# Kernel tuning notes

Hardware: AMD Instinct MI355X
Metric: run time of the kernel (lower is better)

The kernel has to match this reference:

```python
import jax, jax.numpy as jnp
import numpy as np

B, L, D = 8, 2048, 256
D_MODEL = 1024
NUM_SIGNALS = 16
MAX_POSITIONS = 4096
ROLE_OUTPUT = 2  # role id used for the CLS token


def setup_inputs() -> dict:
    key = jax.random.key(0)
    ks = jax.random.split(key, 12)
    emb = jax.random.normal(ks[0], (B, L, D), dtype=jnp.float32)
    pos = jax.random.randint(ks[1], (B, L), 1, MAX_POSITIONS + 1)          # pos >= 1 for real tokens
    sid = jax.random.randint(ks[2], (B, L), 0, NUM_SIGNALS)
    role = jax.random.randint(ks[3], (B, L), 0, 3)
    padding_mask = jax.random.uniform(ks[4], (B, L)) < 0.75                # True = real token
    # learned parameters
    proj_W = jax.random.normal(ks[5], (NUM_SIGNALS, D_MODEL, D), dtype=jnp.float32) * (1.0 / np.sqrt(D))
    proj_b = jax.random.normal(ks[6], (NUM_SIGNALS, D_MODEL), dtype=jnp.float32) * 0.01
    cls_content = jax.random.normal(ks[7], (D_MODEL,), dtype=jnp.float32)
    pos_embed = jax.random.normal(ks[8], (MAX_POSITIONS + 1, D_MODEL), dtype=jnp.float32)
    id_embed = jax.random.normal(ks[9], (NUM_SIGNALS + 1, D_MODEL), dtype=jnp.float32)
    role_embed = jax.random.normal(ks[10], (3, D_MODEL), dtype=jnp.float32)
    return dict(emb=emb, pos=pos, sid=sid, role=role, padding_mask=padding_mask,
                proj_W=proj_W, proj_b=proj_b, cls_content=cls_content,
                pos_embed=pos_embed, id_embed=id_embed, role_embed=role_embed)


def reference(emb, pos, sid, role, padding_mask,
              proj_W, proj_b, cls_content, pos_embed, id_embed, role_embed):
    Bv, Lv, _ = emb.shape
    S, d_model, _ = proj_W.shape
    cls_id = S

    # Grouped per-signal projection: one GEMM per signal id, select per token.
    tokens = jnp.zeros((Bv, Lv, d_model), dtype=emb.dtype)
    for s in range(S):
        proj_s = jnp.einsum('bld,ed->ble', emb, proj_W[s]) + proj_b[s]   # (B, L, d_model)
        keep = ((sid == s) & padding_mask)[..., None]
        tokens = jnp.where(keep, proj_s, tokens)

    # Prepend CLS
    cls = jnp.broadcast_to(cls_content[None, None, :], (Bv, 1, d_model))
    tokens = jnp.concatenate([cls, tokens], axis=1)                       # (B, L+1, d_model)

    pos_full = jnp.concatenate([jnp.zeros((Bv, 1), dtype=pos.dtype), pos], axis=1)
    sid_full = jnp.concatenate([jnp.full((Bv, 1), cls_id, dtype=sid.dtype), sid], axis=1)
    role_full = jnp.concatenate([jnp.full((Bv, 1), ROLE_OUTPUT, dtype=role.dtype), role], axis=1)

    tokens = tokens + pos_embed[pos_full] + id_embed[sid_full] + role_embed[role_full]

    attn_keep = jnp.concatenate([jnp.ones((Bv, 1), dtype=bool), padding_mask], axis=1)
    return tokens, attn_keep
```

## Files before the change

### kernel.cpp

```cpp
#include <hip/hip_runtime.h>
#include <hip/hip_bf16.h>
#include <stdint.h>

#define B_ 8
#define L_ 2048
#define NTOK 16384
#define DK 256
#define DM 1024
#define NS 16
#define LOUT 2049
#define TOK_OUT (B_*LOUT*DM)
#define ATTN_OUT (B_*LOUT)
#define PCAP 2048

typedef unsigned short u16;
typedef unsigned int u32;
typedef __bf16 bf16x8 __attribute__((ext_vector_type(8)));
typedef float f32x4 __attribute__((ext_vector_type(4)));

__device__ inline float bf2f(u16 u) {
    u32 x = ((u32)u) << 16;
    float f;
    __builtin_memcpy(&f, &x, 4);
    return f;
}

__device__ inline u32 packbf2(float lo, float hi) {
    u32 a, b;
    __builtin_memcpy(&a, &lo, 4);
    __builtin_memcpy(&b, &hi, 4);
    a = (a + 0x8000u) >> 16;
    b = (b + 0x8000u) & 0xFFFF0000u;
    return a | b;
}

__device__ inline void gll16(const void* g, void* l) {
    __builtin_amdgcn_global_load_lds(
        (const __attribute__((address_space(1))) unsigned int*)g,
        (__attribute__((address_space(3))) unsigned int*)l, 16, 0, 0);
}

#define WS_CUR 0
#define WS_PERM 64
#define WS_MASK (64 + NS * PCAP)
#define EMB_OFF 262144ULL
#define W_OFF (EMB_OFF + 16384ULL * 512ULL)
#define WS_NEED (W_OFF + 16384ULL * 512ULL)

__global__ __launch_bounds__(256) void prep_all(
    const unsigned char* __restrict__ mb, const int* __restrict__ sid,
    const float* __restrict__ emb, const float* __restrict__ W,
    int* __restrict__ wsi, unsigned char* __restrict__ wsb) {
    __shared__ int f_c1ge2, f_ge2, f_odd;
    __shared__ int lcnt[NS], gbase[NS];
    int bid = blockIdx.x;
    int tid = threadIdx.x;

    if (bid < 64) {
        if (tid == 0) { f_c1ge2 = 0; f_ge2 = 0; f_odd = 0; }
        if (tid < NS) lcnt[tid] = 0;
        __syncthreads();

        int c1ge2 = 0, ge2 = 0, oddnz = 0;
        const u32* mw = (const u32*)mb;
        #pragma unroll
        for (int i = 0; i < 16; i++) {
            u32 x = mw[tid * 16 + i];
            u32 b0 = x & 0xFF, b1 = (x >> 8) & 0xFF, b2 = (x >> 16) & 0xFF, b3 = x >> 24;
            if (b1 >= 2) c1ge2 = 1;
            if (b0 >= 2 || b1 >= 2 || b2 >= 2 || b3 >= 2) ge2 = 1;
            if ((b1 | b3) != 0) oddnz = 1;
        }
        if (c1ge2) atomicOr(&f_c1ge2, 1);
        if (ge2) atomicOr(&f_ge2, 1);
        if (oddnz) atomicOr(&f_odd, 1);
        __syncthreads();

        int width;
        if (f_c1ge2) width = 2;
        else if (f_ge2) width = 4;
        else if (f_odd) width = 1;
        else width = 4;

        int t = bid * 256 + tid;
        int m;
        if (width == 1) m = (mb[t] != 0);
        else if (width == 2) m = (((const u16*)mb)[t] != 0);
        else m = (((const u32*)mb)[t] != 0);

        wsi[WS_MASK + t] = m;
        int s = sid[t];
        int lr = 0;
        if (m) lr = atomicAdd(&lcnt[s], 1);
        __syncthreads();
        if (tid < NS) gbase[tid] = atomicAdd(&wsi[WS_CUR + tid], lcnt[tid]);
        __syncthreads();
        if (m) {
            int r = gbase[s] + lr;
            if (r < PCAP) wsi[WS_PERM + s * PCAP + r] = t;
        }
        return;
    }

    int cb = bid - 64;
    int lane = tid & 63;
    int wv = tid >> 6;
    const float* src;
    u16* dst;
    if (cb < 4096) {
        src = emb;
        dst = (u16*)(wsb + EMB_OFF);
    } else {
        cb -= 4096;
        src = W;
        dst = (u16*)(wsb + W_OFF);
    }
    int r = cb * 4 + wv;
    float4 a = *(const float4*)(src + (size_t)r * DK + lane * 4);
    uint2 o;
    o.x = packbf2(a.x, a.y);
    o.y = packbf2(a.z, a.w);
    *(uint2*)(dst + (size_t)r * DK + lane * 4) = o;
}

__global__ __launch_bounds__(512, 4) void fused_main(
    const int* __restrict__ pos, const int* __restrict__ sid,
    const int* __restrict__ role,
    const float* __restrict__ bias, const float* __restrict__ cls,
    const float* __restrict__ pos_emb, const float* __restrict__ id_emb,
    const float* __restrict__ role_emb,
    const int* __restrict__ wsi, const unsigned char* __restrict__ wsb,
    float* __restrict__ out) {
    __shared__ u16 As[2][128 * 32];
    __shared__ u16 Bs[2][256 * 32];
    __shared__ int toks[128];
    int bi = (int)blockIdx.x;
    int tid = threadIdx.x;
    int lane = tid & 63;
    int wv = tid >> 6;

    if (bi >= 576) {
        int eb = bi - 576;
        if (eb < NTOK / 8) {
            int t = eb * 8 + wv;
            if (wsi[WS_MASK + t]) return;
            int p = pos[t], sd = sid[t], ro = role[t];
            int b = t >> 11, l = t & 2047;
            size_t orow = (size_t)(b * LOUT + l + 1) * DM;
            #pragma unroll
            for (int it = 0; it < 4; it++) {
                int c = it * 256 + lane * 4;
                f32x4 a = *(const f32x4*)(pos_emb + (size_t)p * DM + c);
                f32x4 d = *(const f32x4*)(id_emb + (size_t)sd * DM + c);
                f32x4 e = *(const f32x4*)(role_emb + (size_t)ro * DM + c);
                f32x4 o = a + d + e;
                __builtin_nontemporal_store(o, (f32x4*)(out + orow + c));
            }
        } else if (eb == NTOK / 8) {
            int b = wv;
            size_t orow = (size_t)(b * LOUT) * DM;
            #pragma unroll
            for (int it = 0; it < 4; it++) {
                int c = it * 256 + lane * 4;
                f32x4 cc = *(const f32x4*)(cls + c);
                f32x4 a = *(const f32x4*)(pos_emb + c);
                f32x4 d = *(const f32x4*)(id_emb + NS * DM + c);
                f32x4 e = *(const f32x4*)(role_emb + 2 * DM + c);
                f32x4 o = cc + a + d + e;
                *(f32x4*)(out + orow + c) = o;
            }
        } else {
            int i = (eb - NTOK / 8 - 1) * 512 + tid;
            if (i < ATTN_OUT) {
                int b = i / LOUT;
                int j = i - b * LOUT;
                float val = (j == 0) ? 1.0f : (float)wsi[WS_MASK + b * L_ + j - 1];
                out[TOK_OUT + i] = val;
            }
        }
        return;
    }

    int cnts[NS];
    int mtot = 0;
    #pragma unroll
    for (int i = 0; i < NS; i++) {
        int c = wsi[WS_CUR + i];
        cnts[i] = c > PCAP ? PCAP : c;
        mtot += (cnts[i] + 127) >> 7;
    }
    int xcd = bi & 7;
    int j = bi >> 3;
    int m_lo = (xcd * mtot) >> 3;
    int m_hi = ((xcd + 1) * mtot) >> 3;
    int cm = m_hi - m_lo;
    if (cm <= 0 || j >= cm * 4) return;
    int nt = j / cm;
    int m = m_lo + (j - nt * cm);
    int n0 = nt << 8;

    int s = -1, lrt = 0;
    #pragma unroll
    for (int i = 0; i < NS; i++) {
        int rt = (cnts[i] + 127) >> 7;
        if (s < 0) {
            if (m < rt) { s = i; lrt = m; }
            else m -= rt;
        }
    }
    if (s < 0) return;
    int rowsValid = cnts[s] - lrt * 128;
    if (rowsValid > 128) rowsValid = 128;

    if (tid < 128) {
        int base = WS_PERM + s * PCAP + lrt * 128;
        toks[tid] = wsi[base + ((tid < rowsValid) ? tid : 0)];
    }
    __syncthreads();

    const u16* Eb = (const u16*)(wsb + EMB_OFF);
    const u16* Bb = (const u16*)(wsb + W_OFF) + (size_t)(s * DM + n0) * DK;

    int srow = lane >> 2;
    int slseg = lane & 3;
    int arow = wv * 16 + srow;
    int ags = (slseg - (arow >> 1)) & 3;
    int brow1 = 128 + arow;
    int bgs1 = (slseg - (brow1 >> 1)) & 3;
    const u16* Asrc = Eb + (size_t)toks[arow] * DK;

    f32x4 acc[4][4];
    #pragma unroll
    for (int im = 0; im < 4; im++)
        #pragma unroll
        for (int jn = 0; jn < 4; jn++) acc[im][jn] = (f32x4){0.f, 0.f, 0.f, 0.f};

    int wm = wv & 1, wn = wv >> 1;
    int mcol = lane & 15;
    int quad = lane >> 4;

#define STAGE(kc, bf)                                                          \
    {                                                                          \
        gll16(Asrc + (kc) * 32 + ags * 8, &As[bf][wv * 16 * 32]);              \
        gll16(Bb + (size_t)arow * DK + (kc) * 32 + ags * 8,                    \
              &Bs[bf][wv * 16 * 32]);                                          \
        gll16(Bb + (size_t)brow1 * DK + (kc) * 32 + bgs1 * 8,                  \
              &Bs[bf][(128 + wv * 16) * 32]);                                  \
    }

    STAGE(0, 0)
    #pragma unroll
    for (int kc = 0; kc < 8; ++kc) {
        __syncthreads();
        if (kc < 7) STAGE(kc + 1, (kc + 1) & 1)
        int bf = kc & 1;
        bf16x8 af[4], bfr[4];
        #pragma unroll
        for (int im = 0; im < 4; im++) {
            int row = wm * 64 + im * 16 + mcol;
            int sg = (quad + (row >> 1)) & 3;
            af[im] = *(const bf16x8*)(&As[bf][row * 32 + sg * 8]);
        }
        #pragma unroll
        for (int jn = 0; jn < 4; jn++) {
            int row = wn * 64 + jn * 16 + mcol;
            int sg = (quad + (row >> 1)) & 3;
            bfr[jn] = *(const bf16x8*)(&Bs[bf][row * 32 + sg * 8]);
        }
        #pragma unroll
        for (int im = 0; im < 4; im++)
            #pragma unroll
            for (int jn = 0; jn < 4; jn++)
                acc[im][jn] = __builtin_amdgcn_mfma_f32_16x16x32_bf16(
                    af[im], bfr[jn], acc[im][jn], 0, 0, 0);
    }

    float bc[4];
    #pragma unroll
    for (int jn = 0; jn < 4; jn++) {
        int col = n0 + wn * 64 + jn * 16 + mcol;
        bc[jn] = bias[s * DM + col] + id_emb[s * DM + col];
    }
    #pragma unroll
    for (int im = 0; im < 4; im++) {
        #pragma unroll
        for (int r = 0; r < 4; r++) {
            int rowT = wm * 64 + im * 16 + quad * 4 + r;
            if (rowT >= rowsValid) continue;
            int t = toks[rowT];
            int p = pos[t];
            int ro = role[t];
            int b = t >> 11, l = t & 2047;
            size_t orow = (size_t)(b * LOUT + l + 1) * DM;
            const float* prow = pos_emb + (size_t)p * DM;
            #pragma unroll
            for (int jn = 0; jn < 4; jn++) {
                int col = n0 + wn * 64 + jn * 16 + mcol;
                float val = acc[im][jn][r] + bc[jn]
                    + prow[col]
                    + role_emb[ro * DM + col];
                __builtin_nontemporal_store(val, &out[orow + col]);
            }
        }
    }
#undef STAGE
}

extern "C" void kernel_launch(void* const* d_in, const int* in_sizes, int n_in,
                              void* d_out, int out_size, void* d_ws, size_t ws_size,
                              hipStream_t stream) {
    const float* emb = (const float*)d_in[0];
    const int* pos = (const int*)d_in[1];
    const int* sid = (const int*)d_in[2];
    const int* role = (const int*)d_in[3];
    const unsigned char* mask = (const unsigned char*)d_in[4];
    const float* W = (const float*)d_in[5];
    const float* bias = (const float*)d_in[6];
    const float* cls = (const float*)d_in[7];
    const float* pos_emb = (const float*)d_in[8];
    const float* id_emb = (const float*)d_in[9];
    const float* role_emb = (const float*)d_in[10];
    float* out = (float*)d_out;
    int* wsi = (int*)d_ws;
    unsigned char* wsb = (unsigned char*)d_ws;

    (void)hipMemsetAsync(wsi, 0, 64 * sizeof(int), stream);
    hipLaunchKernelGGL(prep_all, dim3(64 + 8192), dim3(256), 0, stream,
                       mask, sid, emb, W, wsi, wsb);
    hipLaunchKernelGGL(fused_main, dim3(576 + 2048 + 1 + 33), dim3(512), 0, stream,
                       pos, sid, role, bias, cls, pos_emb, id_emb, role_emb,
                       wsi, wsb, out);
}
```

Before: 154.1 us.

## Move masked-token, CLS and attention-mask writes into prep kernel

The elementwise output work (padded-token embedding sums, CLS rows, attention-keep mask) moves out of the GEMM kernel and into the prep kernel. Each of those blocks re-sniffs the mask width on its own, so the workspace mask array is no longer needed. The bf16 conversion blocks now handle four rows per wave instead of one, which cuts the conversion grid from 8192 to 2048 blocks. The aim is to overlap the bandwidth-bound writes with the conversion and leave the second kernel purely GEMM, at the cost of every elementwise block re-reading 16KB of mask.

```diff
diff --git a/kernel.cpp b/kernel.cpp
--- a/kernel.cpp
+++ b/kernel.cpp
@@ -18,13 +18,6 @@
 typedef __bf16 bf16x8 __attribute__((ext_vector_type(8)));
 typedef float f32x4 __attribute__((ext_vector_type(4)));
 
-__device__ inline float bf2f(u16 u) {
-    u32 x = ((u32)u) << 16;
-    float f;
-    __builtin_memcpy(&f, &x, 4);
-    return f;
-}
-
 __device__ inline u32 packbf2(float lo, float hi) {
     u32 a, b;
     __builtin_memcpy(&a, &lo, 4);
@@ -42,53 +35,67 @@
 
 #define WS_CUR 0
 #define WS_PERM 64
-#define WS_MASK (64 + NS * PCAP)
 #define EMB_OFF 262144ULL
 #define W_OFF (EMB_OFF + 16384ULL * 512ULL)
 #define WS_NEED (W_OFF + 16384ULL * 512ULL)
 
+__device__ inline int sniff_width(const unsigned char* mb, int tid, int* sh) {
+    if (tid == 0) { sh[0] = 0; sh[1] = 0; sh[2] = 0; }
+    __syncthreads();
+    int c1ge2 = 0, ge2 = 0, oddnz = 0;
+    const u32* mw = (const u32*)mb;
+    #pragma unroll
+    for (int i = 0; i < 16; i++) {
+        u32 x = mw[tid * 16 + i];
+        u32 b0 = x & 0xFF, b1 = (x >> 8) & 0xFF, b2 = (x >> 16) & 0xFF, b3 = x >> 24;
+        if (b1 >= 2) c1ge2 = 1;
+        if (b0 >= 2 || b1 >= 2 || b2 >= 2 || b3 >= 2) ge2 = 1;
+        if ((b1 | b3) != 0) oddnz = 1;
+    }
+    if (c1ge2) atomicOr(&sh[0], 1);
+    if (ge2) atomicOr(&sh[1], 1);
+    if (oddnz) atomicOr(&sh[2], 1);
+    __syncthreads();
+    if (sh[0]) return 2;
+    if (sh[1]) return 4;
+    if (sh[2]) return 1;
+    return 4;
+}
+
+__device__ inline int decode_mask(const unsigned char* mb, int t, int width) {
+    if (width == 1) return mb[t] != 0;
+    if (width == 2) return ((const u16*)mb)[t] != 0;
+    return ((const u32*)mb)[t] != 0;
+}
+
+#define SORT_B 64
+#define CONV_B 2048
+#define EW_B 4096
+#define EW0 (SORT_B + CONV_B)
+#define CLS0 (EW0 + EW_B)
+#define ATTN0 (CLS0 + 2)
+#define PREP_GRID (ATTN0 + 65)
+
 __global__ __launch_bounds__(256) void prep_all(
     const unsigned char* __restrict__ mb, const int* __restrict__ sid,
+    const int* __restrict__ pos, const int* __restrict__ role,
     const float* __restrict__ emb, const float* __restrict__ W,
-    int* __restrict__ wsi, unsigned char* __restrict__ wsb) {
-    __shared__ int f_c1ge2, f_ge2, f_odd;
+    const float* __restrict__ cls, const float* __restrict__ pos_emb,
+    const float* __restrict__ id_emb, const float* __restrict__ role_emb,
+    int* __restrict__ wsi, unsigned char* __restrict__ wsb,
+    float* __restrict__ out) {
+    __shared__ int sh[3];
     __shared__ int lcnt[NS], gbase[NS];
     int bid = blockIdx.x;
     int tid = threadIdx.x;
-
-    if (bid < 64) {
-        if (tid == 0) { f_c1ge2 = 0; f_ge2 = 0; f_odd = 0; }
+    int lane = tid & 63;
+    int wv = tid >> 6;
+
+    if (bid < SORT_B) {
         if (tid < NS) lcnt[tid] = 0;
-        __syncthreads();
-
-        int c1ge2 = 0, ge2 = 0, oddnz = 0;
-        const u32* mw = (const u32*)mb;
-        #pragma unroll
-        for (int i = 0; i < 16; i++) {
-            u32 x = mw[tid * 16 + i];
-            u32 b0 = x & 0xFF, b1 = (x >> 8) & 0xFF, b2 = (x >> 16) & 0xFF, b3 = x >> 24;
-            if (b1 >= 2) c1ge2 = 1;
-            if (b0 >= 2 || b1 >= 2 || b2 >= 2 || b3 >= 2) ge2 = 1;
-            if ((b1 | b3) != 0) oddnz = 1;
-        }
-        if (c1ge2) atomicOr(&f_c1ge2, 1);
-        if (ge2) atomicOr(&f_ge2, 1);
-        if (oddnz) atomicOr(&f_odd, 1);
-        __syncthreads();
-
-        int width;
-        if (f_c1ge2) width = 2;
-        else if (f_ge2) width = 4;
-        else if (f_odd) width = 1;
-        else width = 4;
-
+        int width = sniff_width(mb, tid, sh);
         int t = bid * 256 + tid;
-        int m;
-        if (width == 1) m = (mb[t] != 0);
-        else if (width == 2) m = (((const u16*)mb)[t] != 0);
-        else m = (((const u32*)mb)[t] != 0);
-
-        wsi[WS_MASK + t] = m;
+        int m = decode_mask(mb, t, width);
         int s = sid[t];
         int lr = 0;
         if (m) lr = atomicAdd(&lcnt[s], 1);
@@ -102,31 +109,85 @@
         return;
     }
 
-    int cb = bid - 64;
-    int lane = tid & 63;
-    int wv = tid >> 6;
-    const float* src;
-    u16* dst;
-    if (cb < 4096) {
-        src = emb;
-        dst = (u16*)(wsb + EMB_OFF);
-    } else {
-        cb -= 4096;
-        src = W;
-        dst = (u16*)(wsb + W_OFF);
-    }
-    int r = cb * 4 + wv;
-    float4 a = *(const float4*)(src + (size_t)r * DK + lane * 4);
-    uint2 o;
-    o.x = packbf2(a.x, a.y);
-    o.y = packbf2(a.z, a.w);
-    *(uint2*)(dst + (size_t)r * DK + lane * 4) = o;
-}
-
-__global__ __launch_bounds__(512, 4) void fused_main(
-    const int* __restrict__ pos, const int* __restrict__ sid,
-    const int* __restrict__ role,
-    const float* __restrict__ bias, const float* __restrict__ cls,
+    if (bid < EW0) {
+        int cb = bid - SORT_B;
+        const float* src;
+        u16* dst;
+        if (cb < 1024) {
+            src = emb;
+            dst = (u16*)(wsb + EMB_OFF);
+        } else {
+            cb -= 1024;
+            src = W;
+            dst = (u16*)(wsb + W_OFF);
+        }
+        int r0 = cb * 16 + wv * 4;
+        #pragma unroll
+        for (int i = 0; i < 4; i++) {
+            int r = r0 + i;
+            float4 a = *(const float4*)(src + (size_t)r * DK + lane * 4);
+            uint2 o;
+            o.x = packbf2(a.x, a.y);
+            o.y = packbf2(a.z, a.w);
+            *(uint2*)(dst + (size_t)r * DK + lane * 4) = o;
+        }
+        return;
+    }
+
+    if (bid < CLS0) {
+        int width = sniff_width(mb, tid, sh);
+        int t = (bid - EW0) * 4 + wv;
+        if (decode_mask(mb, t, width)) return;
+        int p = pos[t], sd = sid[t], ro = role[t];
+        int b = t >> 11, l = t & 2047;
+        size_t orow = (size_t)(b * LOUT + l + 1) * DM;
+        const float* pr = pos_emb + (size_t)p * DM;
+        const float* ir = id_emb + (size_t)sd * DM;
+        const float* rr = role_emb + (size_t)ro * DM;
+        #pragma unroll
+        for (int it = 0; it < 4; it++) {
+            int c = it * 256 + lane * 4;
+            f32x4 a = *(const f32x4*)(pr + c);
+            f32x4 d = *(const f32x4*)(ir + c);
+            f32x4 e = *(const f32x4*)(rr + c);
+            f32x4 o = a + d + e;
+            __builtin_nontemporal_store(o, (f32x4*)(out + orow + c));
+        }
+        return;
+    }
+
+    if (bid < ATTN0) {
+        int b = (bid - CLS0) * 4 + wv;
+        size_t orow = (size_t)(b * LOUT) * DM;
+        #pragma unroll
+        for (int it = 0; it < 4; it++) {
+            int c = it * 256 + lane * 4;
+            f32x4 cc = *(const f32x4*)(cls + c);
+            f32x4 a = *(const f32x4*)(pos_emb + c);
+            f32x4 d = *(const f32x4*)(id_emb + NS * DM + c);
+            f32x4 e = *(const f32x4*)(role_emb + 2 * DM + c);
+            f32x4 o = cc + a + d + e;
+            *(f32x4*)(out + orow + c) = o;
+        }
+        return;
+    }
+
+    {
+        int width = sniff_width(mb, tid, sh);
+        int i = (bid - ATTN0) * 256 + tid;
+        if (i < ATTN_OUT) {
+            int b = i / LOUT;
+            int j = i - b * LOUT;
+            float val = (j == 0) ? 1.0f
+                                 : (float)decode_mask(mb, b * L_ + j - 1, width);
+            out[TOK_OUT + i] = val;
+        }
+    }
+}
+
+__global__ __launch_bounds__(512, 4) void gemm_big(
+    const int* __restrict__ pos, const int* __restrict__ role,
+    const float* __restrict__ bias,
     const float* __restrict__ pos_emb, const float* __restrict__ id_emb,
     const float* __restrict__ role_emb,
     const int* __restrict__ wsi, const unsigned char* __restrict__ wsb,
@@ -138,48 +199,6 @@
     int tid = threadIdx.x;
     int lane = tid & 63;
     int wv = tid >> 6;
-
-    if (bi >= 576) {
-        int eb = bi - 576;
-        if (eb < NTOK / 8) {
-            int t = eb * 8 + wv;
-            if (wsi[WS_MASK + t]) return;
-            int p = pos[t], sd = sid[t], ro = role[t];
-            int b = t >> 11, l = t & 2047;
-            size_t orow = (size_t)(b * LOUT + l + 1) * DM;
-            #pragma unroll
-            for (int it = 0; it < 4; it++) {
-                int c = it * 256 + lane * 4;
-                f32x4 a = *(const f32x4*)(pos_emb + (size_t)p * DM + c);
-                f32x4 d = *(const f32x4*)(id_emb + (size_t)sd * DM + c);
-                f32x4 e = *(const f32x4*)(role_emb + (size_t)ro * DM + c);
-                f32x4 o = a + d + e;
-                __builtin_nontemporal_store(o, (f32x4*)(out + orow + c));
-            }
-        } else if (eb == NTOK / 8) {
-            int b = wv;
-            size_t orow = (size_t)(b * LOUT) * DM;
-            #pragma unroll
-            for (int it = 0; it < 4; it++) {
-                int c = it * 256 + lane * 4;
-                f32x4 cc = *(const f32x4*)(cls + c);
-                f32x4 a = *(const f32x4*)(pos_emb + c);
-                f32x4 d = *(const f32x4*)(id_emb + NS * DM + c);
-                f32x4 e = *(const f32x4*)(role_emb + 2 * DM + c);
-                f32x4 o = cc + a + d + e;
-                *(f32x4*)(out + orow + c) = o;
-            }
-        } else {
-            int i = (eb - NTOK / 8 - 1) * 512 + tid;
-            if (i < ATTN_OUT) {
-                int b = i / LOUT;
-                int j = i - b * LOUT;
-                float val = (j == 0) ? 1.0f : (float)wsi[WS_MASK + b * L_ + j - 1];
-                out[TOK_OUT + i] = val;
-            }
-        }
-        return;
-    }
 
     int cnts[NS];
     int mtot = 0;
@@ -325,9 +344,10 @@
     unsigned char* wsb = (unsigned char*)d_ws;
 
     (void)hipMemsetAsync(wsi, 0, 64 * sizeof(int), stream);
-    hipLaunchKernelGGL(prep_all, dim3(64 + 8192), dim3(256), 0, stream,
-                       mask, sid, emb, W, wsi, wsb);
-    hipLaunchKernelGGL(fused_main, dim3(576 + 2048 + 1 + 33), dim3(512), 0, stream,
-                       pos, sid, role, bias, cls, pos_emb, id_emb, role_emb,
+    hipLaunchKernelGGL(prep_all, dim3(PREP_GRID), dim3(256), 0, stream,
+                       mask, sid, pos, role, emb, W, cls, pos_emb, id_emb,
+                       role_emb, wsi, wsb, out);
+    hipLaunchKernelGGL(gemm_big, dim3(576), dim3(512), 0, stream,
+                       pos, role, bias, pos_emb, id_emb, role_emb,
                        wsi, wsb, out);
 }
```

After: 156.6 us. About the same (+1.6%).
